# Performance work log

Hardware: AMD Instinct MI355X
Metric: run time of the kernel (lower is better)

Reference implementation:

```python
import jax, jax.numpy as jnp
import numpy as np

N, B, H, NH = 16384, 64, 256, 8
MAXN = 512
EPS = 1e-5


def setup_inputs() -> dict:
    key = jax.random.key(0)
    ks = jax.random.split(key, 8)
    s = 0.02
    return {
        "x": jax.random.normal(ks[0], (N, H), jnp.float32),
        "batch": jnp.sort(jax.random.randint(ks[1], (N,), 0, B)),
        "max_nodes": MAXN,
        "norm1_w": jnp.ones((H,), jnp.float32),
        "norm1_b": jnp.zeros((H,), jnp.float32),
        "in_proj_w": jax.random.normal(ks[2], (3 * H, H), jnp.float32) * s,
        "in_proj_b": jnp.zeros((3 * H,), jnp.float32),
        "out_proj_w": jax.random.normal(ks[3], (H, H), jnp.float32) * s,
        "out_proj_b": jnp.zeros((H,), jnp.float32),
        "norm2_w": jnp.ones((H,), jnp.float32),
        "norm2_b": jnp.zeros((H,), jnp.float32),
        "ffn_w1": jax.random.normal(ks[4], (4 * H, H), jnp.float32) * s,
        "ffn_b1": jnp.zeros((4 * H,), jnp.float32),
        "ffn_w2": jax.random.normal(ks[5], (H, 4 * H), jnp.float32) * s,
        "ffn_b2": jnp.zeros((H,), jnp.float32),
    }


def _graph_norm(x, batch, countsf, w, b):
    # Per-graph mean and unbiased std (torch.std default), eps added to std.
    mean = jax.ops.segment_sum(x, batch, num_segments=B) / countsf[:, None]
    c = x - mean[batch]
    var = jax.ops.segment_sum(c * c, batch, num_segments=B) / jnp.maximum(countsf - 1.0, 1.0)[:, None]
    std = jnp.sqrt(var) + EPS
    return w * (c / std[batch]) + b


def _forward(x, batch, max_nodes, norm1_w, norm1_b, in_proj_w, in_proj_b,
             out_proj_w, out_proj_b, norm2_w, norm2_b, ffn_w1, ffn_b1, ffn_w2, ffn_b2):
    n = x.shape[0]
    counts = jax.ops.segment_sum(jnp.ones((n,), jnp.int32), batch, num_segments=B)  # [B]
    countsf = counts.astype(x.dtype)
    starts = jnp.concatenate([jnp.zeros((1,), jnp.int32), jnp.cumsum(counts)[:-1]])
    pos = jnp.arange(n, dtype=jnp.int32) - starts[batch]  # position within graph (batch is sorted)

    # GraphNorm 1, then pack ragged -> padded [B, M, H]
    xn = _graph_norm(x, batch, countsf, norm1_w, norm1_b)
    x_pad = jnp.zeros((B, max_nodes, H), x.dtype).at[batch, pos].set(xn)
    key_valid = jnp.arange(max_nodes)[None, :] < counts[:, None]  # [B, M] True=real node

    # Multi-head attention (eval mode, key_padding_mask)
    qkv = x_pad @ in_proj_w.T + in_proj_b  # [B, M, 3H]
    q, k, v = jnp.split(qkv, 3, axis=-1)
    hd = H // NH
    heads = lambda t: t.reshape(B, max_nodes, NH, hd).transpose(0, 2, 1, 3)  # [B, NH, M, hd]
    q, k, v = heads(q), heads(k), heads(v)
    scores = jnp.einsum('bhqd,bhkd->bhqk', q, k) / np.float32(np.sqrt(hd))
    scores = jnp.where(key_valid[:, None, None, :], scores, jnp.float32(-1e9))
    attn = jax.nn.softmax(scores, axis=-1)
    ctx = jnp.einsum('bhqk,bhkd->bhqd', attn, v).transpose(0, 2, 1, 3).reshape(B, max_nodes, H)
    attn_out = ctx @ out_proj_w.T + out_proj_b

    # Unpack padded -> ragged, residual
    x = x + attn_out[batch, pos]

    # GraphNorm 2 + FFN (exact GELU) + residual
    xn2 = _graph_norm(x, batch, countsf, norm2_w, norm2_b)
    h = jax.nn.gelu(xn2 @ ffn_w1.T + ffn_b1, approximate=False)
    return x + (h @ ffn_w2.T + ffn_b2)


def reference(x, batch, max_nodes, norm1_w, norm1_b, in_proj_w, in_proj_b,
              out_proj_w, out_proj_b, norm2_w, norm2_b, ffn_w1, ffn_b1, ffn_w2, ffn_b2):
    return _forward(x, batch, max_nodes, norm1_w, norm1_b, in_proj_w, in_proj_b,
                    out_proj_w, out_proj_b, norm2_w, norm2_b, ffn_w1, ffn_b1, ffn_w2, ffn_b2)
```

## Files before the change

kernel.cpp:

```cpp
#include <hip/hip_runtime.h>
#include <hip/hip_bf16.h>
#include <math.h>

typedef __bf16 bf16;
typedef bf16 bf16x4 __attribute__((ext_vector_type(4)));
typedef bf16 bf16x8 __attribute__((ext_vector_type(8)));
typedef float f32x4 __attribute__((ext_vector_type(4)));

#define NNODES 16384
#define NB 64
#define HDIM 256
#define NHEADS 8
#define HD 32
#define GN_STRIPS 16

__global__ void meta_kernel(const int* __restrict__ batch, int* __restrict__ starts,
                            int* __restrict__ counts) {
    int b = threadIdx.x;
    if (b >= NB) return;
    int lo = 0, hi = NNODES;
    while (lo < hi) { int mid = (lo + hi) >> 1; if (batch[mid] < b) lo = mid + 1; else hi = mid; }
    int s0 = lo;
    lo = 0; hi = NNODES;
    while (lo < hi) { int mid = (lo + hi) >> 1; if (batch[mid] < b + 1) lo = mid + 1; else hi = mid; }
    starts[b] = s0;
    counts[b] = lo - s0;
}

__global__ void cvt4_kernel(const float* __restrict__ in, bf16* __restrict__ out, int n4) {
    int i = blockIdx.x * 256 + threadIdx.x;
    if (i >= n4) return;
    float4 v = *(const float4*)(in + (size_t)i * 4);
    bf16x4 o;
    o[0] = (bf16)v.x; o[1] = (bf16)v.y; o[2] = (bf16)v.z; o[3] = (bf16)v.w;
    *(bf16x4*)(out + (size_t)i * 4) = o;
}

__global__ __launch_bounds__(256) void gn_partial(
    const float* __restrict__ x, const int* __restrict__ starts,
    const int* __restrict__ counts, float* __restrict__ part) {
    int g = blockIdx.x, strip = blockIdx.y, hh = threadIdx.x;
    int s = starts[g], c = counts[g];
    int chunk = (c + GN_STRIPS - 1) / GN_STRIPS;
    int r0 = strip * chunk, r1 = min(c, r0 + chunk);
    float sum = 0.f, sq = 0.f;
    for (int r = r0; r < r1; ++r) {
        float v = x[(size_t)(s + r) * HDIM + hh];
        sum += v; sq += v * v;
    }
    part[((size_t)(g * GN_STRIPS + strip) * 2 + 0) * HDIM + hh] = sum;
    part[((size_t)(g * GN_STRIPS + strip) * 2 + 1) * HDIM + hh] = sq;
}

__global__ __launch_bounds__(256) void gn_final(
    const float* __restrict__ part, const int* __restrict__ counts,
    const float* __restrict__ w, const float* __restrict__ b, float* __restrict__ stats) {
    int g = blockIdx.x, hh = threadIdx.x;
    float sum = 0.f, sq = 0.f;
    for (int st = 0; st < GN_STRIPS; ++st) {
        sum += part[((size_t)(g * GN_STRIPS + st) * 2 + 0) * HDIM + hh];
        sq  += part[((size_t)(g * GN_STRIPS + st) * 2 + 1) * HDIM + hh];
    }
    float cf = (float)counts[g];
    float mean = sum / cf;
    float var = (sq - cf * mean * mean) / fmaxf(cf - 1.f, 1.f);
    var = fmaxf(var, 0.f);
    float inv = 1.f / (sqrtf(var) + 1e-5f);
    float a = w[hh] * inv;
    stats[(size_t)g * 512 + hh] = a;
    stats[(size_t)g * 512 + 256 + hh] = b[hh] - mean * a;
}

__global__ __launch_bounds__(256) void gn_apply(
    const float* __restrict__ x, const int* __restrict__ batch,
    const float* __restrict__ stats, bf16* __restrict__ out) {
    size_t i = ((size_t)blockIdx.x * 256 + threadIdx.x) * 4;
    int row = (int)(i >> 8);
    int g = batch[row];
    int hh = (int)(i & 255);
    float4 xv = *(const float4*)(x + i);
    float4 av = *(const float4*)(stats + (size_t)g * 512 + hh);
    float4 bv = *(const float4*)(stats + (size_t)g * 512 + 256 + hh);
    bf16x4 o;
    o[0] = (bf16)(av.x * xv.x + bv.x);
    o[1] = (bf16)(av.y * xv.y + bv.y);
    o[2] = (bf16)(av.z * xv.z + bv.z);
    o[3] = (bf16)(av.w * xv.w + bv.w);
    *(bf16x4*)(out + i) = o;
}

template <int MODE>
__global__ __launch_bounds__(256) void gemm_tn(
    const bf16* __restrict__ A, const bf16* __restrict__ B,
    const float* __restrict__ bias, const float* __restrict__ res,
    void* __restrict__ Cout, int M, int N, int K) {
    __shared__ __align__(16) bf16 As[128][40];
    __shared__ __align__(16) bf16 Bs[128][40];
    const int row0 = blockIdx.x * 128;
    const int col0 = blockIdx.y * 128;
    const int tid = threadIdx.x;
    const int lane = tid & 63;
    const int wave = tid >> 6;
    const int wm = (wave >> 1) * 64;
    const int wn = (wave & 1) * 64;
    const int lr = lane & 15;
    const int lk = lane >> 4;
    const int r_st = tid >> 2;
    const int c8_st = (tid & 3) * 8;

    f32x4 acc[4][4] = {};

    for (int k0 = 0; k0 < K; k0 += 32) {
        bf16x8 a0 = *(const bf16x8*)&A[(size_t)(row0 + r_st) * K + k0 + c8_st];
        bf16x8 a1 = *(const bf16x8*)&A[(size_t)(row0 + 64 + r_st) * K + k0 + c8_st];
        bf16x8 b0 = *(const bf16x8*)&B[(size_t)(col0 + r_st) * K + k0 + c8_st];
        bf16x8 b1 = *(const bf16x8*)&B[(size_t)(col0 + 64 + r_st) * K + k0 + c8_st];
        __syncthreads();
        *(bf16x8*)&As[r_st][c8_st] = a0;
        *(bf16x8*)&As[64 + r_st][c8_st] = a1;
        *(bf16x8*)&Bs[r_st][c8_st] = b0;
        *(bf16x8*)&Bs[64 + r_st][c8_st] = b1;
        __syncthreads();
        bf16x8 af[4], bfr[4];
#pragma unroll
        for (int mi = 0; mi < 4; ++mi) af[mi] = *(const bf16x8*)&As[wm + mi * 16 + lr][lk * 8];
#pragma unroll
        for (int ni = 0; ni < 4; ++ni) bfr[ni] = *(const bf16x8*)&Bs[wn + ni * 16 + lr][lk * 8];
#pragma unroll
        for (int mi = 0; mi < 4; ++mi)
#pragma unroll
            for (int ni = 0; ni < 4; ++ni)
                acc[mi][ni] = __builtin_amdgcn_mfma_f32_16x16x32_bf16(af[mi], bfr[ni], acc[mi][ni], 0, 0, 0);
    }

#pragma unroll
    for (int mi = 0; mi < 4; ++mi) {
#pragma unroll
        for (int ni = 0; ni < 4; ++ni) {
            const int col = col0 + wn + ni * 16 + lr;
            const float bv = bias[col];
#pragma unroll
            for (int r = 0; r < 4; ++r) {
                const int row = row0 + wm + mi * 16 + lk * 4 + r;
                float v = acc[mi][ni][r] + bv;
                size_t idx = (size_t)row * N + col;
                if (MODE == 0) {
                    ((bf16*)Cout)[idx] = (bf16)v;
                } else if (MODE == 1) {
                    ((float*)Cout)[idx] = v + res[idx];
                } else {
                    float gel = 0.5f * v * (1.f + erff(v * 0.70710678118654752f));
                    ((bf16*)Cout)[idx] = (bf16)gel;
                }
            }
        }
    }
}

__global__ __launch_bounds__(256) void attn_mfma(
    const bf16* __restrict__ qkv, const int* __restrict__ starts,
    const int* __restrict__ counts, bf16* __restrict__ ctx) {
    int g = blockIdx.x, h = blockIdx.y;
    int s = starts[g], c = counts[g];
    if (c <= 0) return;
    __shared__ __align__(16) bf16 Qs[256][40];
    __shared__ __align__(16) bf16 Ks[64][40];
    __shared__ __align__(16) bf16 Vt[32][72];
    __shared__ __align__(16) bf16 Ps[4][64][72];
    __shared__ float Ls[4][64];
    const int tid = threadIdx.x;
    const int w = tid >> 6, lane = tid & 63;
    const int lo = lane & 15, hi = lane >> 4;
    const float scale = 0.17677669529663687f;
    const int nqc = (c + 255) >> 8;
    const int nkt = (c + 63) >> 6;

    for (int qc = 0; qc < nqc; ++qc) {
        {
            int qrow = qc * 256 + tid;
            const bf16* qp = qkv + (size_t)(s + qrow) * 768 + h * HD;
#pragma unroll
            for (int t4 = 0; t4 < 4; ++t4) {
                bf16x8 sv;
                if (qrow < c) {
                    bf16x8 v = *(const bf16x8*)(qp + t4 * 8);
#pragma unroll
                    for (int u = 0; u < 8; ++u) sv[u] = (bf16)((float)v[u] * scale);
                } else {
#pragma unroll
                    for (int u = 0; u < 8; ++u) sv[u] = (bf16)0.f;
                }
                *(bf16x8*)&Qs[tid][t4 * 8] = sv;
            }
        }
        __syncthreads();
        bf16x8 bq[4];
#pragma unroll
        for (int nt = 0; nt < 4; ++nt) bq[nt] = *(const bf16x8*)&Qs[w * 64 + nt * 16 + lo][hi * 8];

        f32x4 ctxa[4][2] = {};
        float l[4] = {0.f, 0.f, 0.f, 0.f};

        for (int kt = 0; kt < nkt; ++kt) {
            {
                int krow = kt * 64 + (tid >> 2);
                bf16x8 v;
                if (krow < c) v = *(const bf16x8*)(qkv + (size_t)(s + krow) * 768 + 256 + h * HD + (tid & 3) * 8);
                else {
#pragma unroll
                    for (int u = 0; u < 8; ++u) v[u] = (bf16)0.f;
                }
                *(bf16x8*)&Ks[tid >> 2][(tid & 3) * 8] = v;
            }
            {
                int vrow = kt * 64 + (tid & 63);
                int dg = tid >> 6;
                bf16x8 v;
                if (vrow < c) v = *(const bf16x8*)(qkv + (size_t)(s + vrow) * 768 + 512 + h * HD + dg * 8);
                else {
#pragma unroll
                    for (int u = 0; u < 8; ++u) v[u] = (bf16)0.f;
                }
#pragma unroll
                for (int u = 0; u < 8; ++u) Vt[dg * 8 + u][tid & 63] = v[u];
            }
            __syncthreads();

            f32x4 sacc[4][4] = {};
#pragma unroll
            for (int kmt = 0; kmt < 4; ++kmt) {
                bf16x8 ak = *(const bf16x8*)&Ks[kmt * 16 + lo][hi * 8];
#pragma unroll
                for (int nt = 0; nt < 4; ++nt)
                    sacc[kmt][nt] = __builtin_amdgcn_mfma_f32_16x16x32_bf16(ak, bq[nt], sacc[kmt][nt], 0, 0, 0);
            }
#pragma unroll
            for (int kmt = 0; kmt < 4; ++kmt) {
                int kbase = kt * 64 + kmt * 16 + hi * 4;
#pragma unroll
                for (int nt = 0; nt < 4; ++nt) {
                    bf16x4 pv;
#pragma unroll
                    for (int r = 0; r < 4; ++r) {
                        float p = (kbase + r < c) ? __expf(sacc[kmt][nt][r]) : 0.f;
                        l[nt] += p;
                        pv[r] = (bf16)p;
                    }
                    *(bf16x4*)&Ps[w][nt * 16 + lo][kmt * 16 + hi * 4] = pv;
                }
            }
#pragma unroll
            for (int ks = 0; ks < 2; ++ks) {
                bf16x8 bv[2];
#pragma unroll
                for (int dn = 0; dn < 2; ++dn) bv[dn] = *(const bf16x8*)&Vt[dn * 16 + lo][ks * 32 + hi * 8];
#pragma unroll
                for (int qmt = 0; qmt < 4; ++qmt) {
                    bf16x8 ap = *(const bf16x8*)&Ps[w][qmt * 16 + lo][ks * 32 + hi * 8];
#pragma unroll
                    for (int dn = 0; dn < 2; ++dn)
                        ctxa[qmt][dn] = __builtin_amdgcn_mfma_f32_16x16x32_bf16(ap, bv[dn], ctxa[qmt][dn], 0, 0, 0);
                }
            }
            __syncthreads();
        }

#pragma unroll
        for (int nt = 0; nt < 4; ++nt) {
            l[nt] += __shfl_xor(l[nt], 16);
            l[nt] += __shfl_xor(l[nt], 32);
        }
        if (hi == 0) {
#pragma unroll
            for (int nt = 0; nt < 4; ++nt) Ls[w][nt * 16 + lo] = l[nt];
        }
#pragma unroll
        for (int qmt = 0; qmt < 4; ++qmt) {
#pragma unroll
            for (int r = 0; r < 4; ++r) {
                int qrow = qc * 256 + w * 64 + qmt * 16 + hi * 4 + r;
                if (qrow < c) {
                    float linv = 1.f / Ls[w][qmt * 16 + hi * 4 + r];
                    bf16* op = ctx + (size_t)(s + qrow) * HDIM + h * HD;
#pragma unroll
                    for (int dn = 0; dn < 2; ++dn)
                        op[dn * 16 + lo] = (bf16)(ctxa[qmt][dn][r] * linv);
                }
            }
        }
        __syncthreads();
    }
}

extern "C" void kernel_launch(void* const* d_in, const int* in_sizes, int n_in,
                              void* d_out, int out_size, void* d_ws, size_t ws_size,
                              hipStream_t stream) {
    const float* x        = (const float*)d_in[0];
    const int*   batch    = (const int*)d_in[1];
    const float* norm1_w  = (const float*)d_in[3];
    const float* norm1_b  = (const float*)d_in[4];
    const float* in_proj_w  = (const float*)d_in[5];
    const float* in_proj_b  = (const float*)d_in[6];
    const float* out_proj_w = (const float*)d_in[7];
    const float* out_proj_b = (const float*)d_in[8];
    const float* norm2_w  = (const float*)d_in[9];
    const float* norm2_b  = (const float*)d_in[10];
    const float* ffn_w1   = (const float*)d_in[11];
    const float* ffn_b1   = (const float*)d_in[12];
    const float* ffn_w2   = (const float*)d_in[13];
    const float* ffn_b2   = (const float*)d_in[14];
    float* out = (float*)d_out;

    char* ws = (char*)d_ws;
    size_t off = 0;
    auto alloc = [&](size_t bytes) -> void* {
        void* p = ws + off;
        off += bytes;
        off = (off + 255) & ~(size_t)255;
        return p;
    };
    int*  starts = (int*)alloc(NB * 4);
    int*  counts = (int*)alloc(NB * 4);
    bf16* wq = (bf16*)alloc((size_t)768 * 256 * 2);
    bf16* wo = (bf16*)alloc((size_t)256 * 256 * 2);
    bf16* w1 = (bf16*)alloc((size_t)1024 * 256 * 2);
    bf16* w2 = (bf16*)alloc((size_t)256 * 1024 * 2);
    bf16* t0  = (bf16*)alloc((size_t)NNODES * HDIM * 2);
    bf16* qkv = (bf16*)alloc((size_t)NNODES * 768 * 2);
    float* y  = (float*)alloc((size_t)NNODES * HDIM * 4);
    bf16* hbuf = (bf16*)alloc((size_t)NNODES * 1024 * 2);
    float* gnpart = (float*)alloc((size_t)NB * GN_STRIPS * 2 * HDIM * 4);
    float* gnstats = (float*)alloc((size_t)NB * 512 * 4);

    meta_kernel<<<1, 64, 0, stream>>>(batch, starts, counts);
    cvt4_kernel<<<(768 * 256 / 4 + 255) / 256, 256, 0, stream>>>(in_proj_w, wq, 768 * 256 / 4);
    cvt4_kernel<<<(256 * 256 / 4 + 255) / 256, 256, 0, stream>>>(out_proj_w, wo, 256 * 256 / 4);
    cvt4_kernel<<<(1024 * 256 / 4 + 255) / 256, 256, 0, stream>>>(ffn_w1, w1, 1024 * 256 / 4);
    cvt4_kernel<<<(256 * 1024 / 4 + 255) / 256, 256, 0, stream>>>(ffn_w2, w2, 256 * 1024 / 4);
    gn_partial<<<dim3(NB, GN_STRIPS), 256, 0, stream>>>(x, starts, counts, gnpart);
    gn_final<<<NB, 256, 0, stream>>>(gnpart, counts, norm1_w, norm1_b, gnstats);
    gn_apply<<<NNODES * HDIM / 1024, 256, 0, stream>>>(x, batch, gnstats, t0);
    gemm_tn<0><<<dim3(NNODES / 128, 768 / 128), 256, 0, stream>>>(
        t0, wq, in_proj_b, nullptr, qkv, NNODES, 768, 256);
    attn_mfma<<<dim3(NB, NHEADS), 256, 0, stream>>>(qkv, starts, counts, t0);
    gemm_tn<1><<<dim3(NNODES / 128, 256 / 128), 256, 0, stream>>>(
        t0, wo, out_proj_b, x, y, NNODES, 256, 256);
    gn_partial<<<dim3(NB, GN_STRIPS), 256, 0, stream>>>(y, starts, counts, gnpart);
    gn_final<<<NB, 256, 0, stream>>>(gnpart, counts, norm2_w, norm2_b, gnstats);
    gn_apply<<<NNODES * HDIM / 1024, 256, 0, stream>>>(y, batch, gnstats, t0);
    gemm_tn<2><<<dim3(NNODES / 128, 1024 / 128), 256, 0, stream>>>(
        t0, w1, ffn_b1, nullptr, hbuf, NNODES, 1024, 256);
    gemm_tn<1><<<dim3(NNODES / 128, 256 / 128), 256, 0, stream>>>(
        hbuf, w2, ffn_b2, y, out, NNODES, 256, 1024);
}
```

Measured before the change: 251.4 us.

## Use direct global-to-LDS async loads in GEMM and merge weight conversions

The bf16 GEMM now stages its A and B tiles with global_load_lds 16-byte copies straight into shared memory. This skips the register round-trip and the explicit LDS stores, and it drops the row padding so the tile is laid out contiguously as the DMA requires. The four weight-conversion launches are merged into one kernel that picks its source and destination by index range, saving launch overhead. The unpadded 64-byte LDS rows may cause bank conflicts on the fragment reads. The loop is still single-buffered, so loads are not overlapped with MFMA work.

Result: no change. 246.8 us (-1.8%).

```diff
diff --git a/kernel.cpp b/kernel.cpp
--- a/kernel.cpp
+++ b/kernel.cpp
@@ -13,6 +13,13 @@
 #define NHEADS 8
 #define HD 32
 #define GN_STRIPS 16
+
+typedef __attribute__((address_space(3))) unsigned int lds_u32;
+typedef __attribute__((address_space(1))) const unsigned int glb_u32;
+
+__device__ __forceinline__ void async_copy16(const bf16* gsrc, bf16* ldst) {
+    __builtin_amdgcn_global_load_lds((glb_u32*)gsrc, (lds_u32*)ldst, 16, 0, 0);
+}
 
 __global__ void meta_kernel(const int* __restrict__ batch, int* __restrict__ starts,
                             int* __restrict__ counts) {
@@ -27,13 +34,20 @@
     counts[b] = lo - s0;
 }
 
-__global__ void cvt4_kernel(const float* __restrict__ in, bf16* __restrict__ out, int n4) {
+__global__ void cvt_all(const float* __restrict__ pw_q, const float* __restrict__ pw_o,
+                        const float* __restrict__ pw_1, const float* __restrict__ pw_2,
+                        bf16* __restrict__ dq, bf16* __restrict__ dо_unused_pad,
+                        bf16* __restrict__ d_o, bf16* __restrict__ d1, bf16* __restrict__ d2) {
     int i = blockIdx.x * 256 + threadIdx.x;
-    if (i >= n4) return;
-    float4 v = *(const float4*)(in + (size_t)i * 4);
+    const float* src; bf16* dst; int j;
+    if (i < 49152)       { src = pw_q; dst = dq;  j = i; }
+    else if (i < 65536)  { src = pw_o; dst = d_o; j = i - 49152; }
+    else if (i < 131072) { src = pw_1; dst = d1;  j = i - 65536; }
+    else                 { src = pw_2; dst = d2;  j = i - 131072; }
+    float4 v = *(const float4*)(src + (size_t)j * 4);
     bf16x4 o;
     o[0] = (bf16)v.x; o[1] = (bf16)v.y; o[2] = (bf16)v.z; o[3] = (bf16)v.w;
-    *(bf16x4*)(out + (size_t)i * 4) = o;
+    *(bf16x4*)(dst + (size_t)j * 4) = o;
 }
 
 __global__ __launch_bounds__(256) void gn_partial(
@@ -94,8 +108,8 @@
     const bf16* __restrict__ A, const bf16* __restrict__ B,
     const float* __restrict__ bias, const float* __restrict__ res,
     void* __restrict__ Cout, int M, int N, int K) {
-    __shared__ __align__(16) bf16 As[128][40];
-    __shared__ __align__(16) bf16 Bs[128][40];
+    __shared__ __align__(16) bf16 As[128 * 32];
+    __shared__ __align__(16) bf16 Bs[128 * 32];
     const int row0 = blockIdx.x * 128;
     const int col0 = blockIdx.y * 128;
     const int tid = threadIdx.x;
@@ -105,27 +119,30 @@
     const int wn = (wave & 1) * 64;
     const int lr = lane & 15;
     const int lk = lane >> 4;
-    const int r_st = tid >> 2;
-    const int c8_st = (tid & 3) * 8;
+    const int c0 = tid;
+    const int c1 = tid + 256;
+    const int r0c = c0 >> 2, o0 = (c0 & 3) * 8;
+    const int r1c = c1 >> 2, o1 = (c1 & 3) * 8;
+
+    const bf16* Ab = A + (size_t)row0 * K;
+    const bf16* Bb = B + (size_t)col0 * K;
 
     f32x4 acc[4][4] = {};
 
     for (int k0 = 0; k0 < K; k0 += 32) {
-        bf16x8 a0 = *(const bf16x8*)&A[(size_t)(row0 + r_st) * K + k0 + c8_st];
-        bf16x8 a1 = *(const bf16x8*)&A[(size_t)(row0 + 64 + r_st) * K + k0 + c8_st];
-        bf16x8 b0 = *(const bf16x8*)&B[(size_t)(col0 + r_st) * K + k0 + c8_st];
-        bf16x8 b1 = *(const bf16x8*)&B[(size_t)(col0 + 64 + r_st) * K + k0 + c8_st];
         __syncthreads();
-        *(bf16x8*)&As[r_st][c8_st] = a0;
-        *(bf16x8*)&As[64 + r_st][c8_st] = a1;
-        *(bf16x8*)&Bs[r_st][c8_st] = b0;
-        *(bf16x8*)&Bs[64 + r_st][c8_st] = b1;
+        async_copy16(Ab + (size_t)r0c * K + k0 + o0, &As[c0 * 8]);
+        async_copy16(Ab + (size_t)r1c * K + k0 + o1, &As[c1 * 8]);
+        async_copy16(Bb + (size_t)r0c * K + k0 + o0, &Bs[c0 * 8]);
+        async_copy16(Bb + (size_t)r1c * K + k0 + o1, &Bs[c1 * 8]);
         __syncthreads();
         bf16x8 af[4], bfr[4];
 #pragma unroll
-        for (int mi = 0; mi < 4; ++mi) af[mi] = *(const bf16x8*)&As[wm + mi * 16 + lr][lk * 8];
-#pragma unroll
-        for (int ni = 0; ni < 4; ++ni) bfr[ni] = *(const bf16x8*)&Bs[wn + ni * 16 + lr][lk * 8];
+        for (int mi = 0; mi < 4; ++mi)
+            af[mi] = *(const bf16x8*)&As[(wm + mi * 16 + lr) * 32 + lk * 8];
+#pragma unroll
+        for (int ni = 0; ni < 4; ++ni)
+            bfr[ni] = *(const bf16x8*)&Bs[(wn + ni * 16 + lr) * 32 + lk * 8];
 #pragma unroll
         for (int mi = 0; mi < 4; ++mi)
 #pragma unroll
@@ -333,10 +350,8 @@
     float* gnstats = (float*)alloc((size_t)NB * 512 * 4);
 
     meta_kernel<<<1, 64, 0, stream>>>(batch, starts, counts);
-    cvt4_kernel<<<(768 * 256 / 4 + 255) / 256, 256, 0, stream>>>(in_proj_w, wq, 768 * 256 / 4);
-    cvt4_kernel<<<(256 * 256 / 4 + 255) / 256, 256, 0, stream>>>(out_proj_w, wo, 256 * 256 / 4);
-    cvt4_kernel<<<(1024 * 256 / 4 + 255) / 256, 256, 0, stream>>>(ffn_w1, w1, 1024 * 256 / 4);
-    cvt4_kernel<<<(256 * 1024 / 4 + 255) / 256, 256, 0, stream>>>(ffn_w2, w2, 256 * 1024 / 4);
+    cvt_all<<<196608 / 256, 256, 0, stream>>>(in_proj_w, out_proj_w, ffn_w1, ffn_w2,
+                                              wq, nullptr, wo, w1, w2);
     gn_partial<<<dim3(NB, GN_STRIPS), 256, 0, stream>>>(x, starts, counts, gnpart);
     gn_final<<<NB, 256, 0, stream>>>(gnpart, counts, norm1_w, norm1_b, gnstats);
     gn_apply<<<NNODES * HDIM / 1024, 256, 0, stream>>>(x, batch, gnstats, t0);
```
